# Kernel tuning notes

Hardware: AMD Instinct MI355X
Metric: run time of the kernel (lower is better)

Reference implementation:

```python
import jax, jax.numpy as jnp
import numpy as np

B, N, C, H, W = 4, 24, 256, 100, 100
SCALE = 0.25      # feature-map stride scale (MultiScaleRoIAlign spatial scale)
OUT = 7           # output_size
SR = 2            # sampling_ratio
IMG = H / SCALE   # image size in box coordinates (400)


def setup_inputs() -> dict:
    key = jax.random.key(0)
    kf, kx, ky, kw, kh = jax.random.split(key, 5)
    features = jax.random.normal(kf, (B, C, H, W), dtype=jnp.float32)
    # valid boxes: positive height/width (module asserts non-degenerate boxes)
    x1 = jax.random.uniform(kx, (B, N), minval=0.0, maxval=IMG * 0.6)
    y1 = jax.random.uniform(ky, (B, N), minval=0.0, maxval=IMG * 0.6)
    bw = jax.random.uniform(kw, (B, N), minval=16.0, maxval=IMG * 0.35)
    bh = jax.random.uniform(kh, (B, N), minval=16.0, maxval=IMG * 0.35)
    x2 = jnp.minimum(x1 + bw, IMG - 1.0)
    y2 = jnp.minimum(y1 + bh, IMG - 1.0)
    boxes = jnp.stack([x1, y1, x2, y2], axis=-1)  # [B, N, 4] xyxy
    return {"features": features, "boxes": boxes}


def _roi_align(features, rois, batch_ix):
    """torchvision-style RoIAlign (aligned=False). rois: [R,4] xyxy in image coords."""
    R = rois.shape[0]
    x1, y1, x2, y2 = [rois[:, i] * SCALE for i in range(4)]
    roi_w = jnp.maximum(x2 - x1, 1.0)
    roi_h = jnp.maximum(y2 - y1, 1.0)
    bin_w = roi_w / OUT
    bin_h = roi_h / OUT
    # sample-point offsets within the roi: (bin + (k+0.5)/SR) for k in [0,SR)
    grid = (jnp.arange(OUT, dtype=jnp.float32)[:, None]
            + (jnp.arange(SR, dtype=jnp.float32)[None, :] + 0.5) / SR).reshape(-1)  # [OUT*SR]
    ys = y1[:, None] + grid[None, :] * bin_h[:, None]  # [R, 14]
    xs = x1[:, None] + grid[None, :] * bin_w[:, None]  # [R, 14]
    Y = ys[:, :, None]  # [R,14,1]
    X = xs[:, None, :]  # [R,1,14]
    valid = (Y > -1.0) & (Y < H) & (X > -1.0) & (X < W)  # [R,14,14]
    Yc = jnp.clip(Y, 0.0, H - 1.0)
    Xc = jnp.clip(X, 0.0, W - 1.0)
    y0f = jnp.floor(Yc); x0f = jnp.floor(Xc)
    ly = Yc - y0f; lx = Xc - x0f
    hy = 1.0 - ly;  hx = 1.0 - lx
    y0 = y0f.astype(jnp.int32); x0 = x0f.astype(jnp.int32)
    y1i = jnp.minimum(y0 + 1, H - 1); x1i = jnp.minimum(x0 + 1, W - 1)
    b = batch_ix[:, None, None]
    # gathers -> [R,14,14,C] each (advanced indices around the ':' put C last)
    f00 = features[b, :, y0,  x0]
    f01 = features[b, :, y0,  x1i]
    f10 = features[b, :, y1i, x0]
    f11 = features[b, :, y1i, x1i]
    w00 = (hy * hx)[..., None]; w01 = (hy * lx)[..., None]
    w10 = (ly * hx)[..., None]; w11 = (ly * lx)[..., None]
    val = (w00 * f00 + w01 * f01 + w10 * f10 + w11 * f11) * valid[..., None]
    # average SRxSR samples per bin -> [R, OUT, OUT, C] -> [R, C, OUT, OUT]
    pooled = val.reshape(R, OUT, SR, OUT, SR, C).mean(axis=(2, 4))
    return pooled.transpose(0, 3, 1, 2)


def reference(features, boxes):
    # 1) pairwise union boxes (vectorized form of _single_image_expand)
    iu, ju = jnp.triu_indices(N, k=1)          # P pairs, i<j
    b1 = boxes[:, iu]                          # [B, P, 4]
    b2 = boxes[:, ju]
    union = jnp.concatenate([jnp.minimum(b1[..., :2], b2[..., :2]),
                             jnp.maximum(b1[..., 2:], b2[..., 2:])], axis=-1)
    rois = jnp.concatenate([boxes, union], axis=1)  # [B, M, 4], M = N + P
    M = rois.shape[1]
    batch_ix = jnp.repeat(jnp.arange(B), M)
    pooled = _roi_align(features, rois.reshape(-1, 4), batch_ix)  # [B*M, C, 7, 7]
    pooled = pooled.reshape(B, M, C, OUT, OUT)
    # 2) pair assembly (vectorized _ObjPairLayer): [obj_i, obj_j, union_ij]
    obj = pooled[:, :N]    # [B, N, C, 7, 7]
    uni = pooled[:, N:]    # [B, P, C, 7, 7]
    pair_feats = jnp.stack([obj[:, iu], obj[:, ju], uni], axis=2)  # [B, P, 3, C, 7, 7]
    P = iu.shape[0]
    return pair_feats.reshape(B * P, 3, C, OUT, OUT)
```

## Files before the change

kernel.cpp:

```cpp
#include <hip/hip_runtime.h>

#define B_    4
#define N_OBJ 24
#define C_    256
#define H_    100
#define W_    100
#define HW_   (H_ * W_)
#define OUT_  7
#define P_    276
#define M_    (N_OBJ + P_)
#define SCALE_ 0.25f
#define CHW_OUT (C_ * OUT_ * OUT_)

__device__ __forceinline__ void pair_from_p(int p, int& i, int& j) {
    int ii = 0, rem = p;
    while (rem >= N_OBJ - 1 - ii) { rem -= (N_OBJ - 1 - ii); ++ii; }
    i = ii; j = ii + 1 + rem;
}

__global__ __launch_bounds__(256) void transpose_kernel(
        const float* __restrict__ feat, float* __restrict__ featT) {
    __shared__ float tile[64][65];
    const int b   = blockIdx.z;
    const int c0  = blockIdx.y * 64;
    const int px0 = blockIdx.x * 64;
    const int t   = threadIdx.x;
    const int cl  = t >> 6;
    const int px  = t & 63;
#pragma unroll
    for (int k = 0; k < 16; ++k) {
        const int c_loc = cl + k * 4;
        const int gpx   = px0 + px;
        tile[c_loc][px] = (gpx < HW_)
            ? feat[((size_t)b * C_ + c0 + c_loc) * HW_ + gpx] : 0.0f;
    }
    __syncthreads();
    const int c2 = t & 63;
    const int pl = t >> 6;
#pragma unroll
    for (int k = 0; k < 16; ++k) {
        const int px_l = pl + k * 4;
        const int gpx  = px0 + px_l;
        if (gpx < HW_)
            featT[((size_t)b * HW_ + gpx) * C_ + c0 + c2] = tile[c2][px_l];
    }
}

__global__ __launch_bounds__(256) void roi_kernel(
        const float* __restrict__ featT,
        const float* __restrict__ boxes,
        float* __restrict__ out,
        float* __restrict__ ws_obj) {
    __shared__ float lds[CHW_OUT];
    const int r = blockIdx.x;
    const int b = r / M_;
    const int m = r - b * M_;

    float x1, y1, x2, y2;
    if (m < N_OBJ) {
        const float* bp = boxes + ((size_t)b * N_OBJ + m) * 4;
        x1 = bp[0]; y1 = bp[1]; x2 = bp[2]; y2 = bp[3];
    } else {
        int i, j; pair_from_p(m - N_OBJ, i, j);
        const float* b1 = boxes + ((size_t)b * N_OBJ + i) * 4;
        const float* b2 = boxes + ((size_t)b * N_OBJ + j) * 4;
        x1 = fminf(b1[0], b2[0]); y1 = fminf(b1[1], b2[1]);
        x2 = fmaxf(b1[2], b2[2]); y2 = fmaxf(b1[3], b2[3]);
    }
    x1 *= SCALE_; y1 *= SCALE_; x2 *= SCALE_; y2 *= SCALE_;
    const float roi_w = fmaxf(x2 - x1, 1.0f);
    const float roi_h = fmaxf(y2 - y1, 1.0f);
    const float bin_w = roi_w * (1.0f / OUT_);
    const float bin_h = roi_h * (1.0f / OUT_);

    const int lane = threadIdx.x & 63;
    const int wv   = threadIdx.x >> 6;
    const float4* fbase = (const float4*)(featT + (size_t)b * HW_ * C_) + lane;

    for (int s = wv; s < OUT_ * OUT_; s += 4) {
        const int ph = s / OUT_, pw = s - ph * OUT_;
        float4 acc = make_float4(0.f, 0.f, 0.f, 0.f);
#pragma unroll
        for (int iy = 0; iy < 2; ++iy) {
            const float Y  = y1 + ((float)ph + (iy ? 0.75f : 0.25f)) * bin_h;
            const bool vy  = (Y > -1.0f) && (Y < (float)H_);
            const float Yc = fminf(fmaxf(Y, 0.0f), (float)(H_ - 1));
            const int  y0  = (int)floorf(Yc);
            const float ly = Yc - (float)y0;
            const float hy = 1.0f - ly;
            const int  y1i = min(y0 + 1, H_ - 1);
#pragma unroll
            for (int ix = 0; ix < 2; ++ix) {
                const float X  = x1 + ((float)pw + (ix ? 0.75f : 0.25f)) * bin_w;
                const bool vx  = (X > -1.0f) && (X < (float)W_);
                const float Xc = fminf(fmaxf(X, 0.0f), (float)(W_ - 1));
                const int  x0  = (int)floorf(Xc);
                const float lx = Xc - (float)x0;
                const float hx = 1.0f - lx;
                const int  x1i = min(x0 + 1, W_ - 1);
                const float vs = (vy && vx) ? 0.25f : 0.0f;
                const float w00 = vs * hy * hx, w01 = vs * hy * lx;
                const float w10 = vs * ly * hx, w11 = vs * ly * lx;
                const float4 f00 = fbase[(y0  * W_ + x0 ) * (C_ / 4)];
                const float4 f01 = fbase[(y0  * W_ + x1i) * (C_ / 4)];
                const float4 f10 = fbase[(y1i * W_ + x0 ) * (C_ / 4)];
                const float4 f11 = fbase[(y1i * W_ + x1i) * (C_ / 4)];
                acc.x += w00 * f00.x + w01 * f01.x + w10 * f10.x + w11 * f11.x;
                acc.y += w00 * f00.y + w01 * f01.y + w10 * f10.y + w11 * f11.y;
                acc.z += w00 * f00.z + w01 * f01.z + w10 * f10.z + w11 * f11.z;
                acc.w += w00 * f00.w + w01 * f01.w + w10 * f10.w + w11 * f11.w;
            }
        }
        const int c0 = lane * 4;
        lds[(c0 + 0) * 49 + s] = acc.x;
        lds[(c0 + 1) * 49 + s] = acc.y;
        lds[(c0 + 2) * 49 + s] = acc.z;
        lds[(c0 + 3) * 49 + s] = acc.w;
    }
    __syncthreads();

    float* dst = (m < N_OBJ)
        ? (ws_obj + ((size_t)b * N_OBJ + m) * CHW_OUT)
        : (out + (((size_t)(b * P_ + (m - N_OBJ))) * 3 + 2) * CHW_OUT);
    const float4* s4 = (const float4*)lds;
    float4* d4 = (float4*)dst;
    for (int idx = threadIdx.x; idx < CHW_OUT / 4; idx += 256)
        d4[idx] = s4[idx];
}

__global__ __launch_bounds__(256) void assemble_kernel(
        const float* __restrict__ ws_obj, float* __restrict__ out) {
    const int bp   = blockIdx.x;
    const int slot = blockIdx.y;
    const int b = bp / P_;
    const int p = bp - b * P_;
    int i, j; pair_from_p(p, i, j);
    const int n = slot ? j : i;
    const float4* src = (const float4*)(ws_obj + ((size_t)b * N_OBJ + n) * CHW_OUT);
    float4* dst = (float4*)(out + (((size_t)bp) * 3 + slot) * CHW_OUT);
    for (int idx = threadIdx.x; idx < CHW_OUT / 4; idx += 256)
        dst[idx] = src[idx];
}

extern "C" void kernel_launch(void* const* d_in, const int* in_sizes, int n_in,
                              void* d_out, int out_size, void* d_ws, size_t ws_size,
                              hipStream_t stream) {
    const float* feat  = (const float*)d_in[0];
    const float* boxes = (const float*)d_in[1];
    float* out = (float*)d_out;

    float* featT  = (float*)d_ws;
    float* ws_obj = featT + (size_t)B_ * HW_ * C_;

    transpose_kernel<<<dim3((HW_ + 63) / 64, C_ / 64, B_), 256, 0, stream>>>(feat, featT);
    roi_kernel<<<B_ * M_, 256, 0, stream>>>(featT, boxes, out, ws_obj);
    assemble_kernel<<<dim3(B_ * P_, 2), 256, 0, stream>>>(ws_obj, out);
}
```

Baseline: 276.1 us.

## Fuse transpose, RoI align and pair assembly into one persistent kernel with grid barriers

Result: slower. 478.8 us (+73.4%).

```diff
diff --git a/kernel.cpp b/kernel.cpp
--- a/kernel.cpp
+++ b/kernel.cpp
@@ -11,6 +11,12 @@
 #define M_    (N_OBJ + P_)
 #define SCALE_ 0.25f
 #define CHW_OUT (C_ * OUT_ * OUT_)
+#define GRID_ 768
+#define NTHR_ 256
+
+#define PX_TILES   ((HW_ + 63) / 64)
+#define T_TILES    (B_ * (C_ / 64) * PX_TILES)
+#define CP_JOBS    (B_ * P_ * 2)
 
 __device__ __forceinline__ void pair_from_p(int p, int& i, int& j) {
     int ii = 0, rem = p;
@@ -18,128 +24,154 @@
     i = ii; j = ii + 1 + rem;
 }
 
-__global__ __launch_bounds__(256) void transpose_kernel(
-        const float* __restrict__ feat, float* __restrict__ featT) {
-    __shared__ float tile[64][65];
-    const int b   = blockIdx.z;
-    const int c0  = blockIdx.y * 64;
-    const int px0 = blockIdx.x * 64;
-    const int t   = threadIdx.x;
-    const int cl  = t >> 6;
-    const int px  = t & 63;
-#pragma unroll
-    for (int k = 0; k < 16; ++k) {
-        const int c_loc = cl + k * 4;
-        const int gpx   = px0 + px;
-        tile[c_loc][px] = (gpx < HW_)
-            ? feat[((size_t)b * C_ + c0 + c_loc) * HW_ + gpx] : 0.0f;
+__device__ __forceinline__ void grid_barrier(unsigned* bar) {
+    __syncthreads();
+    if (threadIdx.x == 0) {
+        __threadfence();
+        unsigned g = __hip_atomic_load(bar + 1, __ATOMIC_RELAXED, __HIP_MEMORY_SCOPE_AGENT);
+        unsigned arrived = __hip_atomic_fetch_add(bar, 1u, __ATOMIC_RELAXED, __HIP_MEMORY_SCOPE_AGENT);
+        if (arrived == GRID_ - 1) {
+            __hip_atomic_store(bar, 0u, __ATOMIC_RELAXED, __HIP_MEMORY_SCOPE_AGENT);
+            __hip_atomic_fetch_add(bar + 1, 1u, __ATOMIC_RELEASE, __HIP_MEMORY_SCOPE_AGENT);
+        } else {
+            while (__hip_atomic_load(bar + 1, __ATOMIC_RELAXED, __HIP_MEMORY_SCOPE_AGENT) == g)
+                __builtin_amdgcn_s_sleep(2);
+        }
+        __threadfence();
     }
     __syncthreads();
-    const int c2 = t & 63;
-    const int pl = t >> 6;
-#pragma unroll
-    for (int k = 0; k < 16; ++k) {
-        const int px_l = pl + k * 4;
-        const int gpx  = px0 + px_l;
-        if (gpx < HW_)
-            featT[((size_t)b * HW_ + gpx) * C_ + c0 + c2] = tile[c2][px_l];
-    }
 }
 
-__global__ __launch_bounds__(256) void roi_kernel(
-        const float* __restrict__ featT,
+__global__ __launch_bounds__(NTHR_, 3) void fused_kernel(
+        const float* __restrict__ feat,
         const float* __restrict__ boxes,
         float* __restrict__ out,
-        float* __restrict__ ws_obj) {
+        float* __restrict__ featT,
+        float* __restrict__ ws_obj,
+        unsigned* __restrict__ bar) {
     __shared__ float lds[CHW_OUT];
-    const int r = blockIdx.x;
-    const int b = r / M_;
-    const int m = r - b * M_;
+    const int t = threadIdx.x;
 
-    float x1, y1, x2, y2;
-    if (m < N_OBJ) {
-        const float* bp = boxes + ((size_t)b * N_OBJ + m) * 4;
-        x1 = bp[0]; y1 = bp[1]; x2 = bp[2]; y2 = bp[3];
-    } else {
-        int i, j; pair_from_p(m - N_OBJ, i, j);
-        const float* b1 = boxes + ((size_t)b * N_OBJ + i) * 4;
-        const float* b2 = boxes + ((size_t)b * N_OBJ + j) * 4;
-        x1 = fminf(b1[0], b2[0]); y1 = fminf(b1[1], b2[1]);
-        x2 = fmaxf(b1[2], b2[2]); y2 = fmaxf(b1[3], b2[3]);
-    }
-    x1 *= SCALE_; y1 *= SCALE_; x2 *= SCALE_; y2 *= SCALE_;
-    const float roi_w = fmaxf(x2 - x1, 1.0f);
-    const float roi_h = fmaxf(y2 - y1, 1.0f);
-    const float bin_w = roi_w * (1.0f / OUT_);
-    const float bin_h = roi_h * (1.0f / OUT_);
-
-    const int lane = threadIdx.x & 63;
-    const int wv   = threadIdx.x >> 6;
-    const float4* fbase = (const float4*)(featT + (size_t)b * HW_ * C_) + lane;
-
-    for (int s = wv; s < OUT_ * OUT_; s += 4) {
-        const int ph = s / OUT_, pw = s - ph * OUT_;
-        float4 acc = make_float4(0.f, 0.f, 0.f, 0.f);
+    {
+        float (*tile)[65] = (float (*)[65])lds;
+        for (int tl = blockIdx.x; tl < T_TILES; tl += GRID_) {
+            const int b    = tl / ((C_ / 64) * PX_TILES);
+            const int rem  = tl - b * ((C_ / 64) * PX_TILES);
+            const int c0   = (rem / PX_TILES) * 64;
+            const int px0  = (rem - (rem / PX_TILES) * PX_TILES) * 64;
+            const int cl   = t >> 6;
+            const int px   = t & 63;
+            __syncthreads();
 #pragma unroll
-        for (int iy = 0; iy < 2; ++iy) {
-            const float Y  = y1 + ((float)ph + (iy ? 0.75f : 0.25f)) * bin_h;
-            const bool vy  = (Y > -1.0f) && (Y < (float)H_);
-            const float Yc = fminf(fmaxf(Y, 0.0f), (float)(H_ - 1));
-            const int  y0  = (int)floorf(Yc);
-            const float ly = Yc - (float)y0;
-            const float hy = 1.0f - ly;
-            const int  y1i = min(y0 + 1, H_ - 1);
+            for (int k = 0; k < 16; ++k) {
+                const int c_loc = cl + k * 4;
+                const int gpx   = px0 + px;
+                tile[c_loc][px] = (gpx < HW_)
+                    ? feat[((size_t)b * C_ + c0 + c_loc) * HW_ + gpx] : 0.0f;
+            }
+            __syncthreads();
+            const int c2 = t & 63;
+            const int pl = t >> 6;
 #pragma unroll
-            for (int ix = 0; ix < 2; ++ix) {
-                const float X  = x1 + ((float)pw + (ix ? 0.75f : 0.25f)) * bin_w;
-                const bool vx  = (X > -1.0f) && (X < (float)W_);
-                const float Xc = fminf(fmaxf(X, 0.0f), (float)(W_ - 1));
-                const int  x0  = (int)floorf(Xc);
-                const float lx = Xc - (float)x0;
-                const float hx = 1.0f - lx;
-                const int  x1i = min(x0 + 1, W_ - 1);
-                const float vs = (vy && vx) ? 0.25f : 0.0f;
-                const float w00 = vs * hy * hx, w01 = vs * hy * lx;
-                const float w10 = vs * ly * hx, w11 = vs * ly * lx;
-                const float4 f00 = fbase[(y0  * W_ + x0 ) * (C_ / 4)];
-                const float4 f01 = fbase[(y0  * W_ + x1i) * (C_ / 4)];
-                const float4 f10 = fbase[(y1i * W_ + x0 ) * (C_ / 4)];
-                const float4 f11 = fbase[(y1i * W_ + x1i) * (C_ / 4)];
-                acc.x += w00 * f00.x + w01 * f01.x + w10 * f10.x + w11 * f11.x;
-                acc.y += w00 * f00.y + w01 * f01.y + w10 * f10.y + w11 * f11.y;
-                acc.z += w00 * f00.z + w01 * f01.z + w10 * f10.z + w11 * f11.z;
-                acc.w += w00 * f00.w + w01 * f01.w + w10 * f10.w + w11 * f11.w;
+            for (int k = 0; k < 16; ++k) {
+                const int px_l = pl + k * 4;
+                const int gpx  = px0 + px_l;
+                if (gpx < HW_)
+                    featT[((size_t)b * HW_ + gpx) * C_ + c0 + c2] = tile[c2][px_l];
             }
         }
-        const int c0 = lane * 4;
-        lds[(c0 + 0) * 49 + s] = acc.x;
-        lds[(c0 + 1) * 49 + s] = acc.y;
-        lds[(c0 + 2) * 49 + s] = acc.z;
-        lds[(c0 + 3) * 49 + s] = acc.w;
     }
-    __syncthreads();
+    grid_barrier(bar);
 
-    float* dst = (m < N_OBJ)
-        ? (ws_obj + ((size_t)b * N_OBJ + m) * CHW_OUT)
-        : (out + (((size_t)(b * P_ + (m - N_OBJ))) * 3 + 2) * CHW_OUT);
-    const float4* s4 = (const float4*)lds;
-    float4* d4 = (float4*)dst;
-    for (int idx = threadIdx.x; idx < CHW_OUT / 4; idx += 256)
-        d4[idx] = s4[idx];
-}
+    {
+        const int lane = t & 63;
+        const int wv   = t >> 6;
+        for (int r = blockIdx.x; r < B_ * M_; r += GRID_) {
+            const int b = r / M_;
+            const int m = r - b * M_;
 
-__global__ __launch_bounds__(256) void assemble_kernel(
-        const float* __restrict__ ws_obj, float* __restrict__ out) {
-    const int bp   = blockIdx.x;
-    const int slot = blockIdx.y;
-    const int b = bp / P_;
-    const int p = bp - b * P_;
-    int i, j; pair_from_p(p, i, j);
-    const int n = slot ? j : i;
-    const float4* src = (const float4*)(ws_obj + ((size_t)b * N_OBJ + n) * CHW_OUT);
-    float4* dst = (float4*)(out + (((size_t)bp) * 3 + slot) * CHW_OUT);
-    for (int idx = threadIdx.x; idx < CHW_OUT / 4; idx += 256)
-        dst[idx] = src[idx];
+            float x1, y1, x2, y2;
+            if (m < N_OBJ) {
+                const float* bp = boxes + ((size_t)b * N_OBJ + m) * 4;
+                x1 = bp[0]; y1 = bp[1]; x2 = bp[2]; y2 = bp[3];
+            } else {
+                int i, j; pair_from_p(m - N_OBJ, i, j);
+                const float* b1 = boxes + ((size_t)b * N_OBJ + i) * 4;
+                const float* b2 = boxes + ((size_t)b * N_OBJ + j) * 4;
+                x1 = fminf(b1[0], b2[0]); y1 = fminf(b1[1], b2[1]);
+                x2 = fmaxf(b1[2], b2[2]); y2 = fmaxf(b1[3], b2[3]);
+            }
+            x1 *= SCALE_; y1 *= SCALE_; x2 *= SCALE_; y2 *= SCALE_;
+            const float bin_w = fmaxf(x2 - x1, 1.0f) * (1.0f / OUT_);
+            const float bin_h = fmaxf(y2 - y1, 1.0f) * (1.0f / OUT_);
+
+            const float4* fbase = (const float4*)(featT + (size_t)b * HW_ * C_) + lane;
+            __syncthreads();
+            for (int s = wv; s < OUT_ * OUT_; s += 4) {
+                const int ph = s / OUT_, pw = s - ph * OUT_;
+                float4 acc = make_float4(0.f, 0.f, 0.f, 0.f);
+#pragma unroll
+                for (int iy = 0; iy < 2; ++iy) {
+                    const float Y  = y1 + ((float)ph + (iy ? 0.75f : 0.25f)) * bin_h;
+                    const bool vy  = (Y > -1.0f) && (Y < (float)H_);
+                    const float Yc = fminf(fmaxf(Y, 0.0f), (float)(H_ - 1));
+                    const int  y0  = (int)floorf(Yc);
+                    const float ly = Yc - (float)y0;
+                    const float hy = 1.0f - ly;
+                    const int  y1i = min(y0 + 1, H_ - 1);
+#pragma unroll
+                    for (int ix = 0; ix < 2; ++ix) {
+                        const float X  = x1 + ((float)pw + (ix ? 0.75f : 0.25f)) * bin_w;
+                        const bool vx  = (X > -1.0f) && (X < (float)W_);
+                        const float Xc = fminf(fmaxf(X, 0.0f), (float)(W_ - 1));
+                        const int  x0  = (int)floorf(Xc);
+                        const float lx = Xc - (float)x0;
+                        const float hx = 1.0f - lx;
+                        const int  x1i = min(x0 + 1, W_ - 1);
+                        const float vs = (vy && vx) ? 0.25f : 0.0f;
+                        const float w00 = vs * hy * hx, w01 = vs * hy * lx;
+                        const float w10 = vs * ly * hx, w11 = vs * ly * lx;
+                        const float4 f00 = fbase[(y0  * W_ + x0 ) * (C_ / 4)];
+                        const float4 f01 = fbase[(y0  * W_ + x1i) * (C_ / 4)];
+                        const float4 f10 = fbase[(y1i * W_ + x0 ) * (C_ / 4)];
+                        const float4 f11 = fbase[(y1i * W_ + x1i) * (C_ / 4)];
+                        acc.x += w00 * f00.x + w01 * f01.x + w10 * f10.x + w11 * f11.x;
+                        acc.y += w00 * f00.y + w01 * f01.y + w10 * f10.y + w11 * f11.y;
+                        acc.z += w00 * f00.z + w01 * f01.z + w10 * f10.z + w11 * f11.z;
+                        acc.w += w00 * f00.w + w01 * f01.w + w10 * f10.w + w11 * f11.w;
+                    }
+                }
+                const int c0 = lane * 4;
+                lds[(c0 + 0) * 49 + s] = acc.x;
+                lds[(c0 + 1) * 49 + s] = acc.y;
+                lds[(c0 + 2) * 49 + s] = acc.z;
+                lds[(c0 + 3) * 49 + s] = acc.w;
+            }
+            __syncthreads();
+
+            float* dst = (m < N_OBJ)
+                ? (ws_obj + ((size_t)b * N_OBJ + m) * CHW_OUT)
+                : (out + (((size_t)(b * P_ + (m - N_OBJ))) * 3 + 2) * CHW_OUT);
+            const float4* s4 = (const float4*)lds;
+            float4* d4 = (float4*)dst;
+            for (int idx = t; idx < CHW_OUT / 4; idx += NTHR_)
+                d4[idx] = s4[idx];
+        }
+    }
+    grid_barrier(bar);
+
+    for (int job = blockIdx.x; job < CP_JOBS; job += GRID_) {
+        const int slot = job & 1;
+        const int bp   = job >> 1;
+        const int b = bp / P_;
+        const int p = bp - b * P_;
+        int i, j; pair_from_p(p, i, j);
+        const int n = slot ? j : i;
+        const float4* src = (const float4*)(ws_obj + ((size_t)b * N_OBJ + n) * CHW_OUT);
+        float4* dst = (float4*)(out + (((size_t)bp) * 3 + slot) * CHW_OUT);
+        for (int idx = t; idx < CHW_OUT / 4; idx += NTHR_)
+            dst[idx] = src[idx];
+    }
 }
 
 extern "C" void kernel_launch(void* const* d_in, const int* in_sizes, int n_in,
@@ -151,8 +183,8 @@
 
     float* featT  = (float*)d_ws;
     float* ws_obj = featT + (size_t)B_ * HW_ * C_;
+    unsigned* bar = (unsigned*)(ws_obj + (size_t)B_ * N_OBJ * CHW_OUT);
 
-    transpose_kernel<<<dim3((HW_ + 63) / 64, C_ / 64, B_), 256, 0, stream>>>(feat, featT);
-    roi_kernel<<<B_ * M_, 256, 0, stream>>>(featT, boxes, out, ws_obj);
-    assemble_kernel<<<dim3(B_ * P_, 2), 256, 0, stream>>>(ws_obj, out);
+    (void)hipMemsetAsync(bar, 0, 2 * sizeof(unsigned), stream);
+    fused_kernel<<<GRID_, NTHR_, 0, stream>>>(feat, boxes, out, featT, ws_obj, bar);
 }
```

## Remap ROI blocks to XCDs per batch, batch gathers, use nontemporal stores

Applied to the files above, without the earlier changes.

Measured after the change: 252.1 us. 8.7% less time.

```diff
diff --git a/kernel.cpp b/kernel.cpp
--- a/kernel.cpp
+++ b/kernel.cpp
@@ -11,6 +11,8 @@
 #define M_    (N_OBJ + P_)
 #define SCALE_ 0.25f
 #define CHW_OUT (C_ * OUT_ * OUT_)
+
+typedef float f4_t __attribute__((ext_vector_type(4)));
 
 __device__ __forceinline__ void pair_from_p(int p, int& i, int& j) {
     int ii = 0, rem = p;
@@ -52,9 +54,9 @@
         float* __restrict__ out,
         float* __restrict__ ws_obj) {
     __shared__ float lds[CHW_OUT];
-    const int r = blockIdx.x;
-    const int b = r / M_;
-    const int m = r - b * M_;
+    const int xcd = blockIdx.x & 7;
+    const int b   = xcd >> 1;
+    const int m   = ((blockIdx.x >> 3) << 1) | (xcd & 1);
 
     float x1, y1, x2, y2;
     if (m < N_OBJ) {
@@ -68,49 +70,53 @@
         x2 = fmaxf(b1[2], b2[2]); y2 = fmaxf(b1[3], b2[3]);
     }
     x1 *= SCALE_; y1 *= SCALE_; x2 *= SCALE_; y2 *= SCALE_;
-    const float roi_w = fmaxf(x2 - x1, 1.0f);
-    const float roi_h = fmaxf(y2 - y1, 1.0f);
-    const float bin_w = roi_w * (1.0f / OUT_);
-    const float bin_h = roi_h * (1.0f / OUT_);
+    const float bin_w = fmaxf(x2 - x1, 1.0f) * (1.0f / OUT_);
+    const float bin_h = fmaxf(y2 - y1, 1.0f) * (1.0f / OUT_);
 
     const int lane = threadIdx.x & 63;
     const int wv   = threadIdx.x >> 6;
-    const float4* fbase = (const float4*)(featT + (size_t)b * HW_ * C_) + lane;
+    const f4_t* fbase = (const f4_t*)(featT + (size_t)b * HW_ * C_) + lane;
 
     for (int s = wv; s < OUT_ * OUT_; s += 4) {
         const int ph = s / OUT_, pw = s - ph * OUT_;
-        float4 acc = make_float4(0.f, 0.f, 0.f, 0.f);
+
+        float ywt[2][2]; int yi[2][2];
 #pragma unroll
         for (int iy = 0; iy < 2; ++iy) {
             const float Y  = y1 + ((float)ph + (iy ? 0.75f : 0.25f)) * bin_h;
-            const bool vy  = (Y > -1.0f) && (Y < (float)H_);
+            const float vy = (Y > -1.0f && Y < (float)H_) ? 1.0f : 0.0f;
             const float Yc = fminf(fmaxf(Y, 0.0f), (float)(H_ - 1));
             const int  y0  = (int)floorf(Yc);
             const float ly = Yc - (float)y0;
-            const float hy = 1.0f - ly;
-            const int  y1i = min(y0 + 1, H_ - 1);
+            yi[iy][0] = y0; yi[iy][1] = min(y0 + 1, H_ - 1);
+            ywt[iy][0] = vy * (1.0f - ly); ywt[iy][1] = vy * ly;
+        }
+        float xwt[2][2]; int xi[2][2];
 #pragma unroll
-            for (int ix = 0; ix < 2; ++ix) {
-                const float X  = x1 + ((float)pw + (ix ? 0.75f : 0.25f)) * bin_w;
-                const bool vx  = (X > -1.0f) && (X < (float)W_);
-                const float Xc = fminf(fmaxf(X, 0.0f), (float)(W_ - 1));
-                const int  x0  = (int)floorf(Xc);
-                const float lx = Xc - (float)x0;
-                const float hx = 1.0f - lx;
-                const int  x1i = min(x0 + 1, W_ - 1);
-                const float vs = (vy && vx) ? 0.25f : 0.0f;
-                const float w00 = vs * hy * hx, w01 = vs * hy * lx;
-                const float w10 = vs * ly * hx, w11 = vs * ly * lx;
-                const float4 f00 = fbase[(y0  * W_ + x0 ) * (C_ / 4)];
-                const float4 f01 = fbase[(y0  * W_ + x1i) * (C_ / 4)];
-                const float4 f10 = fbase[(y1i * W_ + x0 ) * (C_ / 4)];
-                const float4 f11 = fbase[(y1i * W_ + x1i) * (C_ / 4)];
-                acc.x += w00 * f00.x + w01 * f01.x + w10 * f10.x + w11 * f11.x;
-                acc.y += w00 * f00.y + w01 * f01.y + w10 * f10.y + w11 * f11.y;
-                acc.z += w00 * f00.z + w01 * f01.z + w10 * f10.z + w11 * f11.z;
-                acc.w += w00 * f00.w + w01 * f01.w + w10 * f10.w + w11 * f11.w;
-            }
+        for (int ix = 0; ix < 2; ++ix) {
+            const float X  = x1 + ((float)pw + (ix ? 0.75f : 0.25f)) * bin_w;
+            const float vx = (X > -1.0f && X < (float)W_) ? 0.25f : 0.0f;
+            const float Xc = fminf(fmaxf(X, 0.0f), (float)(W_ - 1));
+            const int  x0  = (int)floorf(Xc);
+            const float lx = Xc - (float)x0;
+            xi[ix][0] = x0; xi[ix][1] = min(x0 + 1, W_ - 1);
+            xwt[ix][0] = vx * (1.0f - lx); xwt[ix][1] = vx * lx;
         }
+
+        int   offs[16]; float wts[16];
+#pragma unroll
+        for (int k = 0; k < 16; ++k) {
+            const int iy = k >> 3, ix = (k >> 2) & 1, cy = (k >> 1) & 1, cx = k & 1;
+            offs[k] = (yi[iy][cy] * W_ + xi[ix][cx]) * (C_ / 4);
+            wts[k]  = ywt[iy][cy] * xwt[ix][cx];
+        }
+        f4_t f[16];
+#pragma unroll
+        for (int k = 0; k < 16; ++k) f[k] = fbase[offs[k]];
+        f4_t acc = (f4_t){0.f, 0.f, 0.f, 0.f};
+#pragma unroll
+        for (int k = 0; k < 16; ++k) acc += wts[k] * f[k];
+
         const int c0 = lane * 4;
         lds[(c0 + 0) * 49 + s] = acc.x;
         lds[(c0 + 1) * 49 + s] = acc.y;
@@ -119,13 +125,16 @@
     }
     __syncthreads();
 
-    float* dst = (m < N_OBJ)
-        ? (ws_obj + ((size_t)b * N_OBJ + m) * CHW_OUT)
-        : (out + (((size_t)(b * P_ + (m - N_OBJ))) * 3 + 2) * CHW_OUT);
-    const float4* s4 = (const float4*)lds;
-    float4* d4 = (float4*)dst;
-    for (int idx = threadIdx.x; idx < CHW_OUT / 4; idx += 256)
-        d4[idx] = s4[idx];
+    const f4_t* s4 = (const f4_t*)lds;
+    if (m < N_OBJ) {
+        f4_t* d4 = (f4_t*)(ws_obj + ((size_t)b * N_OBJ + m) * CHW_OUT);
+        for (int idx = threadIdx.x; idx < CHW_OUT / 4; idx += 256)
+            d4[idx] = s4[idx];
+    } else {
+        f4_t* d4 = (f4_t*)(out + (((size_t)(b * P_ + (m - N_OBJ))) * 3 + 2) * CHW_OUT);
+        for (int idx = threadIdx.x; idx < CHW_OUT / 4; idx += 256)
+            __builtin_nontemporal_store(s4[idx], d4 + idx);
+    }
 }
 
 __global__ __launch_bounds__(256) void assemble_kernel(
@@ -136,10 +145,10 @@
     const int p = bp - b * P_;
     int i, j; pair_from_p(p, i, j);
     const int n = slot ? j : i;
-    const float4* src = (const float4*)(ws_obj + ((size_t)b * N_OBJ + n) * CHW_OUT);
-    float4* dst = (float4*)(out + (((size_t)bp) * 3 + slot) * CHW_OUT);
+    const f4_t* src = (const f4_t*)(ws_obj + ((size_t)b * N_OBJ + n) * CHW_OUT);
+    f4_t* dst = (f4_t*)(out + (((size_t)bp) * 3 + slot) * CHW_OUT);
     for (int idx = threadIdx.x; idx < CHW_OUT / 4; idx += 256)
-        dst[idx] = src[idx];
+        __builtin_nontemporal_store(src[idx], dst + idx);
 }
 
 extern "C" void kernel_launch(void* const* d_in, const int* in_sizes, int n_in,
```
